# Kernel tuning notes

Measured on AMD Instinct MI355X. Metric: run time of the kernel, lower is better.

## Reference

```python
import jax, jax.numpy as jnp
import numpy as np

EPS = 1e-5


def _ln(x, g, b):
    m = jnp.mean(x, axis=-1, keepdims=True)
    v = jnp.var(x, axis=-1, keepdims=True)
    return (x - m) * jax.lax.rsqrt(v + EPS) * g + b


def setup_inputs() -> dict:
    key = jax.random.key(0)
    B, N, C, H = 1, 384, 128, 128
    ks = jax.random.split(key, 8)

    def lin(k, fan_in, fan_out):
        return (jax.random.normal(k, (fan_in, fan_out), jnp.float32)
                / np.float32(np.sqrt(fan_in)))

    return {
        "pair": jax.random.normal(ks[0], (B, N, N, C), jnp.float32),
        # LayerNorm params
        "g_left": jnp.ones((C,), jnp.float32), "b_left": jnp.zeros((C,), jnp.float32),
        "g_right": jnp.ones((C,), jnp.float32), "b_right": jnp.zeros((C,), jnp.float32),
        "g_out": jnp.ones((C,), jnp.float32), "b_out": jnp.zeros((C,), jnp.float32),
        # Linear params (stored as (in, out))
        "W_l": lin(ks[1], C, H), "bias_l": jnp.zeros((H,), jnp.float32),
        "W_r": lin(ks[2], C, H), "bias_r": jnp.zeros((H,), jnp.float32),
        "W_g": lin(ks[3], C, H), "bias_g": jnp.zeros((H,), jnp.float32),
        "W_e": lin(ks[4], C, H), "bias_e": jnp.zeros((H,), jnp.float32),
        "W_o": lin(ks[5], H, C), "bias_o": jnp.zeros((C,), jnp.float32),
    }


def reference(pair, g_left, b_left, g_right, b_right, g_out, b_out,
              W_l, bias_l, W_r, bias_r, W_g, bias_g, W_e, bias_e,
              W_o, bias_o):
    # pair: (B, N, N, C)
    left = _ln(pair, g_left, b_left) @ W_l + bias_l        # (B,N,N,H)
    right = _ln(pair, g_right, b_right) @ W_r + bias_r     # (B,N,N,H)
    gate = jax.nn.sigmoid(pair @ W_g + bias_g)             # (B,N,N,H)
    left = left + pair @ W_e + bias_e                      # eq branch
    # triangular multiplication: contract over k per hidden channel
    out = jnp.einsum('bikh,bkjh->bijh', left, right)       # (B,N,N,H)
    out = out * gate
    out = out @ W_o + bias_o                               # (B,N,N,C)
    return _ln(out + pair, g_out, b_out)
```

## Files before the change

### kernel.cpp

```cpp
#include <hip/hip_runtime.h>

#define N_  384
#define C_  128
#define NN_ (N_*N_)

typedef __bf16 bf16x8 __attribute__((ext_vector_type(8)));
typedef float  floatx4 __attribute__((ext_vector_type(4)));

__device__ inline unsigned short f2bf(float f) {
    __bf16 h = (__bf16)f;
    return __builtin_bit_cast(unsigned short, h);
}

__global__ void prep(
    const float* __restrict__ Wl, const float* __restrict__ Wr,
    const float* __restrict__ Wg, const float* __restrict__ We,
    const float* __restrict__ gl, const float* __restrict__ bl,
    const float* __restrict__ gr, const float* __restrict__ br,
    const float* __restrict__ bsl, const float* __restrict__ bse,
    const float* __restrict__ bsr,
    __bf16* __restrict__ WtL, __bf16* __restrict__ WtE,
    __bf16* __restrict__ WtR, __bf16* __restrict__ WtG,
    float* __restrict__ cL, float* __restrict__ cR,
    float* __restrict__ sEw, float* __restrict__ sGw)
{
    const int b = blockIdx.x, t = threadIdx.x;
    if (b < 4) {
        const float* W  = (b==0) ? Wl  : (b==1) ? We  : (b==2) ? Wr  : Wg;
        __bf16*      Wt = (b==0) ? WtL : (b==1) ? WtE : (b==2) ? WtR : WtG;
        float scale = (b==0) ? gl[t] : (b==2) ? gr[t] : 1.f;
        for (int h = 0; h < C_; ++h)
            Wt[(size_t)h*C_ + t] = (__bf16)(W[(size_t)t*C_ + h] * scale);
    } else {
        float aL = 0.f, aR = 0.f, aE = 0.f, aG = 0.f;
        for (int c = 0; c < C_; ++c) {
            aL += bl[c] * Wl[(size_t)c*C_ + t];
            aR += br[c] * Wr[(size_t)c*C_ + t];
            aE += We[(size_t)c*C_ + t];
            aG += Wg[(size_t)c*C_ + t];
        }
        cL[t]  = aL + bsl[t] + bse[t];
        cR[t]  = aR + bsr[t];
        sEw[t] = aE;
        sGw[t] = aG;
    }
}

__global__ __launch_bounds__(256) void p_proj(
    const float* __restrict__ pair,
    const __bf16* __restrict__ WtL, const __bf16* __restrict__ WtE,
    const __bf16* __restrict__ WtR, const __bf16* __restrict__ WtG,
    const float* __restrict__ cL, const float* __restrict__ cR,
    const float* __restrict__ sEw, const float* __restrict__ sGw,
    const float* __restrict__ bsg,
    int h0, int nh,
    __bf16* __restrict__ leftC, __bf16* __restrict__ rightC,
    __bf16* __restrict__ gateC)
{
    __shared__ __align__(16) __bf16 sW4[4][32][128];
    __shared__ __align__(16) __bf16 sT3[3][32][72];
    __shared__ float sM[64], sIv[64];

    const int t = threadIdx.x;
    const int rid0 = blockIdx.x * 64;
    const int lane = t & 63, w = t >> 6;
    const int l15 = lane & 15, quad = lane >> 4;

    bf16x8 yf[4];
    {
        const int myrow = w*16 + l15;
        const float* prow = pair + (size_t)(rid0 + myrow)*C_;
        float4 xa[4], xb[4];
        float s = 0.f, sq = 0.f;
        #pragma unroll
        for (int ks = 0; ks < 4; ++ks) {
            xa[ks] = *(const float4*)(prow + ks*32 + quad*8);
            xb[ks] = *(const float4*)(prow + ks*32 + quad*8 + 4);
            s  += xa[ks].x + xa[ks].y + xa[ks].z + xa[ks].w
                + xb[ks].x + xb[ks].y + xb[ks].z + xb[ks].w;
            sq += xa[ks].x*xa[ks].x + xa[ks].y*xa[ks].y
                + xa[ks].z*xa[ks].z + xa[ks].w*xa[ks].w
                + xb[ks].x*xb[ks].x + xb[ks].y*xb[ks].y
                + xb[ks].z*xb[ks].z + xb[ks].w*xb[ks].w;
        }
        s  += __shfl_xor(s, 16);  s  += __shfl_xor(s, 32);
        sq += __shfl_xor(sq, 16); sq += __shfl_xor(sq, 32);
        float m  = s * (1.f/128.f);
        float v  = sq * (1.f/128.f) - m*m;
        float rs = rsqrtf(v + 1e-5f);
        if (quad == 0) { sM[myrow] = m; sIv[myrow] = 1.f / rs; }
        #pragma unroll
        for (int ks = 0; ks < 4; ++ks) {
            yf[ks][0] = (__bf16)((xa[ks].x - m)*rs);
            yf[ks][1] = (__bf16)((xa[ks].y - m)*rs);
            yf[ks][2] = (__bf16)((xa[ks].z - m)*rs);
            yf[ks][3] = (__bf16)((xa[ks].w - m)*rs);
            yf[ks][4] = (__bf16)((xb[ks].x - m)*rs);
            yf[ks][5] = (__bf16)((xb[ks].y - m)*rs);
            yf[ks][6] = (__bf16)((xb[ks].z - m)*rs);
            yf[ks][7] = (__bf16)((xb[ks].w - m)*rs);
        }
    }

    for (int half = 0; half < nh; ++half) {
        const int hb = h0 + half*32;
        {
            const int hh = t >> 3, c8 = t & 7;
            const __bf16* srcs[4] = {
                WtL + (size_t)(hb + hh)*C_, WtE + (size_t)(hb + hh)*C_,
                WtR + (size_t)(hb + hh)*C_, WtG + (size_t)(hb + hh)*C_ };
            #pragma unroll
            for (int mat = 0; mat < 4; ++mat) {
                #pragma unroll
                for (int rep = 0; rep < 2; ++rep) {
                    int cc = c8 + rep*8;
                    *(uint4*)&sW4[mat][hh][((cc ^ (hh & 7)) << 3)] =
                        *(const uint4*)(srcs[mat] + cc*8);
                }
            }
        }
        __syncthreads();

        floatx4 aL[2] = {}, aE[2] = {}, aR[2] = {}, aG[2] = {};
        #pragma unroll
        for (int ks = 0; ks < 4; ++ks) {
            const int cs = ((ks*4 + quad) ^ (l15 & 7)) << 3;
            const bf16x8 af = yf[ks];
            #pragma unroll
            for (int nt = 0; nt < 2; ++nt) {
                const int hr = nt*16 + l15;
                aL[nt] = __builtin_amdgcn_mfma_f32_16x16x32_bf16(
                    af, *(const bf16x8*)&sW4[0][hr][cs], aL[nt], 0, 0, 0);
                aE[nt] = __builtin_amdgcn_mfma_f32_16x16x32_bf16(
                    af, *(const bf16x8*)&sW4[1][hr][cs], aE[nt], 0, 0, 0);
                aR[nt] = __builtin_amdgcn_mfma_f32_16x16x32_bf16(
                    af, *(const bf16x8*)&sW4[2][hr][cs], aR[nt], 0, 0, 0);
                aG[nt] = __builtin_amdgcn_mfma_f32_16x16x32_bf16(
                    af, *(const bf16x8*)&sW4[3][hr][cs], aG[nt], 0, 0, 0);
            }
        }

        #pragma unroll
        for (int nt = 0; nt < 2; ++nt) {
            const int hl_ = nt*16 + l15;
            const float se = sEw[hb + hl_], clv = cL[hb + hl_];
            const float crv = cR[hb + hl_];
            const float sg_ = sGw[hb + hl_], bg = bsg[hb + hl_];
            #pragma unroll
            for (int reg = 0; reg < 4; ++reg) {
                const int rr = w*16 + quad*4 + reg;
                sT3[0][hl_][rr] = (__bf16)(aL[nt][reg] + sIv[rr]*aE[nt][reg]
                                           + sM[rr]*se + clv);
                sT3[1][hl_][rr] = (__bf16)(aR[nt][reg] + crv);
                float z = sIv[rr]*aG[nt][reg] + sM[rr]*sg_ + bg;
                sT3[2][hl_][rr] = (__bf16)(1.f / (1.f + expf(-z)));
            }
        }
        __syncthreads();
        {
            const int hh = t >> 3, sg = t & 7;
            const size_t off = (size_t)(half*32 + hh)*NN_ + rid0 + sg*8;
            *(uint4*)(leftC  + off) = *(const uint4*)&sT3[0][hh][sg*8];
            *(uint4*)(rightC + off) = *(const uint4*)&sT3[1][hh][sg*8];
            *(uint4*)(gateC  + off) = *(const uint4*)&sT3[2][hh][sg*8];
        }
        if (half + 1 < nh) __syncthreads();
    }
}

__global__ __launch_bounds__(256) void t_right(__bf16* __restrict__ p)
{
    __shared__ __align__(16) __bf16 tA[64][72];
    __shared__ __align__(16) __bf16 tB[64][72];
    const int plane = blockIdx.x / 21;
    int rem = blockIdx.x % 21, ri = 0;
    while (rem >= 6 - ri) { rem -= 6 - ri; ++ri; }
    const int ci = ri + rem;
    __bf16* base = p + (size_t)plane * NN_;
    const int t = threadIdx.x;
    const int r = t >> 2, c0 = (t & 3) * 16;

    {
        const __bf16* srcA = base + (size_t)(ri*64 + r)*N_ + ci*64 + c0;
        *(uint4*)&tA[r][c0]   = *(const uint4*)(srcA);
        *(uint4*)&tA[r][c0+8] = *(const uint4*)(srcA + 8);
        if (ri != ci) {
            const __bf16* srcB = base + (size_t)(ci*64 + r)*N_ + ri*64 + c0;
            *(uint4*)&tB[r][c0]   = *(const uint4*)(srcB);
            *(uint4*)&tB[r][c0+8] = *(const uint4*)(srcB + 8);
        }
    }
    __syncthreads();
    {
        union { unsigned short us[8]; uint4 v; } o0, o1;
        #pragma unroll
        for (int u = 0; u < 8; ++u) {
            o0.us[u] = __builtin_bit_cast(unsigned short, tA[c0+u][r]);
            o1.us[u] = __builtin_bit_cast(unsigned short, tA[c0+8+u][r]);
        }
        __bf16* dA = base + (size_t)(ci*64 + r)*N_ + ri*64 + c0;
        *(uint4*)(dA)     = o0.v;
        *(uint4*)(dA + 8) = o1.v;
        if (ri != ci) {
            union { unsigned short us[8]; uint4 v; } p0, p1;
            #pragma unroll
            for (int u = 0; u < 8; ++u) {
                p0.us[u] = __builtin_bit_cast(unsigned short, tB[c0+u][r]);
                p1.us[u] = __builtin_bit_cast(unsigned short, tB[c0+8+u][r]);
            }
            __bf16* dB = base + (size_t)(ri*64 + r)*N_ + ci*64 + c0;
            *(uint4*)(dB)     = p0.v;
            *(uint4*)(dB + 8) = p1.v;
        }
    }
}

__global__ __launch_bounds__(256) void k_einsum(
    const __bf16* __restrict__ leftC, const __bf16* __restrict__ rightC,
    const __bf16* __restrict__ gate, __bf16* __restrict__ outG)
{
    __shared__ __align__(16) unsigned char smem[128*136*2];
    __bf16 (*sA)[40]    = (__bf16(*)[40])smem;
    __bf16 (*sB)[40]    = (__bf16(*)[40])(smem + 128*40*2);
    __bf16 (*sGate)[136] = (__bf16(*)[136])smem;

    const int cpx = gridDim.x >> 3;
    const int bid = (blockIdx.x & 7) * cpx + (blockIdx.x >> 3);
    const int hl = bid / 9, t9 = bid % 9;
    const int ti = (t9 / 3) * 128, tj = (t9 % 3) * 128;
    const int tid = threadIdx.x, lane = tid & 63, w = tid >> 6;
    const int l15 = lane & 15, quad = lane >> 4;
    const size_t hNN = (size_t)hl * NN_;

    const int ar = (lane >> 2);
    const int ac = (lane & 3) * 8;
    const __bf16* gA = leftC  + hNN + (size_t)ti * N_;
    const __bf16* gB = rightC + hNN + (size_t)tj * N_;

    floatx4 acc[4][4] = {};

    for (int ks = 0; ks < 12; ++ks) {
        const int kc = ks * 32;
        uint4 va[2], vb[2];
        #pragma unroll
        for (int it = 0; it < 2; ++it) {
            int row = w*32 + it*16 + ar;
            va[it] = *(const uint4*)(gA + (size_t)row*N_ + kc + ac);
            vb[it] = *(const uint4*)(gB + (size_t)row*N_ + kc + ac);
        }
        #pragma unroll
        for (int it = 0; it < 2; ++it) {
            int row = w*32 + it*16 + ar;
            *(uint4*)&sA[row][ac] = va[it];
            *(uint4*)&sB[row][ac] = vb[it];
        }
        __syncthreads();
        bf16x8 af[4], bfr[4];
        #pragma unroll
        for (int mt = 0; mt < 4; ++mt)
            af[mt] = *(const bf16x8*)&sA[(w&1)*64 + mt*16 + l15][quad*8];
        #pragma unroll
        for (int nt = 0; nt < 4; ++nt)
            bfr[nt] = *(const bf16x8*)&sB[(w>>1)*64 + nt*16 + l15][quad*8];
        #pragma unroll
        for (int mt = 0; mt < 4; ++mt)
            #pragma unroll
            for (int nt = 0; nt < 4; ++nt)
                acc[mt][nt] = __builtin_amdgcn_mfma_f32_16x16x32_bf16(
                    af[mt], bfr[nt], acc[mt][nt], 0, 0, 0);
        __syncthreads();
    }

    #pragma unroll
    for (int it = 0; it < 8; ++it) {
        int cid = it*256 + tid;
        int ri = cid >> 4, c8 = cid & 15;
        *(uint4*)&sGate[ri][c8*8] =
            *(const uint4*)(gate + hNN + (size_t)(ti + ri)*N_ + tj + c8*8);
    }
    __syncthreads();

    const int ib = (w & 1) * 64, jbw = (w >> 1) * 64;
    #pragma unroll
    for (int mt = 0; mt < 4; ++mt) {
        const int i_base = ib + mt*16 + quad*4;
        #pragma unroll
        for (int nt = 0; nt < 4; ++nt) {
            const int j_loc = jbw + nt*16 + l15;
            union { unsigned short us[4]; uint2 v; } p;
            #pragma unroll
            for (int rr = 0; rr < 4; ++rr) {
                float g = (float)sGate[i_base + rr][j_loc];
                p.us[rr] = f2bf(acc[mt][nt][rr] * g);
            }
            *(uint2*)(outG + hNN + (size_t)(tj + j_loc)*N_ + ti + i_base) = p.v;
        }
    }
}

__global__ __launch_bounds__(256) void p_out(
    const __bf16* __restrict__ outG, const float* __restrict__ Wo,
    const float* __restrict__ bso,  const float* __restrict__ pair,
    const float* __restrict__ go,   const float* __restrict__ bo,
    float* __restrict__ out)
{
    __shared__ __align__(16) __bf16 sOh[64][128];
    __shared__ __align__(16) __bf16 sWo[128][128];

    const int t = threadIdx.x;
    const int j  = blockIdx.x / 6;
    const int i0 = (blockIdx.x % 6) * 64;
    const int lane = t & 63, w = t >> 6;
    const int l15 = lane & 15, quad = lane >> 4;

    {
        const int h = t >> 1, ibase = (t & 1) * 32;
        const __bf16* src = outG + (size_t)h*NN_ + (size_t)j*N_ + i0 + ibase;
        #pragma unroll
        for (int u = 0; u < 4; ++u) {
            uint4 vv = *(const uint4*)(src + u*8);
            const unsigned short* pv = (const unsigned short*)&vv;
            #pragma unroll
            for (int k = 0; k < 8; ++k) {
                int i = ibase + u*8 + k;
                sOh[i][(((h >> 3) ^ (i & 7)) << 3) + (h & 7)] =
                    __builtin_bit_cast(__bf16, pv[k]);
            }
        }
    }
    {
        const int h = t >> 1, cbase = (t & 1) * 64;
        const float* src = Wo + (size_t)h*C_ + cbase;
        #pragma unroll
        for (int u = 0; u < 16; ++u) {
            float4 wv = *(const float4*)(src + u*4);
            const float* wf = (const float*)&wv;
            #pragma unroll
            for (int k = 0; k < 4; ++k) {
                int c = cbase + u*4 + k;
                sWo[c][(((h >> 3) ^ (c & 7)) << 3) + (h & 7)] = (__bf16)wf[k];
            }
        }
    }
    __syncthreads();

    floatx4 acc[8] = {};
    #pragma unroll
    for (int ks = 0; ks < 4; ++ks) {
        const int cs = ((ks*4 + quad) ^ (l15 & 7)) << 3;
        bf16x8 af = *(const bf16x8*)&sOh[w*16 + l15][cs];
        #pragma unroll
        for (int nt = 0; nt < 8; ++nt)
            acc[nt] = __builtin_amdgcn_mfma_f32_16x16x32_bf16(
                af, *(const bf16x8*)&sWo[nt*16 + l15][cs], acc[nt], 0, 0, 0);
    }

    float bsov[8], gov[8], bov[8];
    #pragma unroll
    for (int nt = 0; nt < 8; ++nt) {
        const int c = nt*16 + l15;
        bsov[nt] = bso[c]; gov[nt] = go[c]; bov[nt] = bo[c];
    }

    #pragma unroll
    for (int reg = 0; reg < 4; ++reg) {
        const int i = i0 + w*16 + quad*4 + reg;
        const float* prow = pair + ((size_t)i*N_ + j)*C_;
        float zz[8];
        float ssum = 0.f, ssq = 0.f;
        #pragma unroll
        for (int nt = 0; nt < 8; ++nt) {
            float zv = acc[nt][reg] + bsov[nt] + prow[nt*16 + l15];
            zz[nt] = zv; ssum += zv; ssq += zv*zv;
        }
        #pragma unroll
        for (int d = 1; d < 16; d <<= 1) {
            ssum += __shfl_xor(ssum, d);
            ssq  += __shfl_xor(ssq, d);
        }
        const float mm = ssum * (1.f/128.f);
        const float vv = ssq * (1.f/128.f) - mm*mm;
        const float rr = rsqrtf(vv + 1e-5f);
        float* orow = out + ((size_t)i*N_ + j)*C_;
        #pragma unroll
        for (int nt = 0; nt < 8; ++nt)
            orow[nt*16 + l15] = (zz[nt] - mm)*rr*gov[nt] + bov[nt];
    }
}

extern "C" void kernel_launch(void* const* d_in, const int* in_sizes, int n_in,
                              void* d_out, int out_size, void* d_ws, size_t ws_size,
                              hipStream_t stream)
{
    const float* pair    = (const float*)d_in[0];
    const float* g_left  = (const float*)d_in[1];
    const float* b_left  = (const float*)d_in[2];
    const float* g_right = (const float*)d_in[3];
    const float* b_right = (const float*)d_in[4];
    const float* g_out   = (const float*)d_in[5];
    const float* b_out   = (const float*)d_in[6];
    const float* W_l     = (const float*)d_in[7];
    const float* bias_l  = (const float*)d_in[8];
    const float* W_r     = (const float*)d_in[9];
    const float* bias_r  = (const float*)d_in[10];
    const float* W_g     = (const float*)d_in[11];
    const float* bias_g  = (const float*)d_in[12];
    const float* W_e     = (const float*)d_in[13];
    const float* bias_e  = (const float*)d_in[14];
    const float* W_o     = (const float*)d_in[15];
    const float* bias_o  = (const float*)d_in[16];

    const size_t PLANES128 = (size_t)128 * NN_;
    const size_t NEED = PLANES128*2*2 + 65536*2 + 512*4;

    if (ws_size >= NEED) {
        __bf16* leftC  = (__bf16*)d_out;
        __bf16* gateC  = leftC + PLANES128;
        __bf16* rightC = (__bf16*)d_ws;
        __bf16* outG   = rightC + PLANES128;
        char* prepBase = (char*)d_ws + PLANES128*2*2;
        __bf16* WtL = (__bf16*)prepBase;
        __bf16* WtE = WtL + 16384;
        __bf16* WtR = WtL + 32768;
        __bf16* WtG = WtL + 49152;
        float*  cL  = (float*)(WtL + 65536);
        float*  cR  = cL + 128;
        float*  sEw = cL + 256;
        float*  sGw = cL + 384;

        prep<<<5, 128, 0, stream>>>(W_l, W_r, W_g, W_e,
                                    g_left, b_left, g_right, b_right,
                                    bias_l, bias_e, bias_r,
                                    WtL, WtE, WtR, WtG, cL, cR, sEw, sGw);
        p_proj<<<NN_/64, 256, 0, stream>>>(pair, WtL, WtE, WtR, WtG,
                                           cL, cR, sEw, sGw, bias_g,
                                           0, 4, leftC, rightC, gateC);
        t_right<<<128*21, 256, 0, stream>>>(rightC);
        k_einsum<<<128*9, 256, 0, stream>>>(leftC, rightC, gateC, outG);
        p_out<<<2304, 256, 0, stream>>>(outG, W_o, bias_o, pair,
                                        g_out, b_out, (float*)d_out);
    } else {
        __bf16* outG   = (__bf16*)d_ws;
        __bf16* leftC  = (__bf16*)d_out;
        __bf16* rightC = leftC + (size_t)64*NN_;
        __bf16* gateC  = leftC + (size_t)128*NN_;

        char* prepBase = (char*)d_out + ((size_t)60 << 20);
        __bf16* WtL = (__bf16*)prepBase;
        __bf16* WtE = WtL + 16384;
        __bf16* WtR = WtL + 32768;
        __bf16* WtG = WtL + 49152;
        float*  cL  = (float*)(WtL + 65536);
        float*  cR  = cL + 128;
        float*  sEw = cL + 256;
        float*  sGw = cL + 384;

        prep<<<5, 128, 0, stream>>>(W_l, W_r, W_g, W_e,
                                    g_left, b_left, g_right, b_right,
                                    bias_l, bias_e, bias_r,
                                    WtL, WtE, WtR, WtG, cL, cR, sEw, sGw);

        for (int h0 = 0; h0 < 128; h0 += 64) {
            p_proj<<<NN_/64, 256, 0, stream>>>(pair, WtL, WtE, WtR, WtG,
                                               cL, cR, sEw, sGw, bias_g,
                                               h0, 2, leftC, rightC, gateC);
            t_right<<<64*21, 256, 0, stream>>>(rightC);
            k_einsum<<<64*9, 256, 0, stream>>>(leftC, rightC, gateC,
                                               outG + (size_t)h0*NN_);
        }
        p_out<<<2304, 256, 0, stream>>>(outG, W_o, bias_o, pair,
                                        g_out, b_out, (float*)d_out);
    }
}
```

Measured before the change: 293.8 us.

## Prefetch next weight and K-tile loads into registers to overlap with MFMA

In the projection kernel, the weights for the next 32-channel chunk are loaded into registers before the current chunk's MFMAs and written to shared memory after the stores, which removes one barrier per iteration. In the triangular matmul kernel, the global loads for the next K-slice are issued after the barrier and before the MFMA block, so memory latency overlaps with compute. The sigmoid also switches from expf to the faster __expf intrinsic. The cost is extra register pressure, which may lower occupancy, plus slightly reduced accuracy in the sigmoid.

```diff
diff --git a/kernel.cpp b/kernel.cpp
--- a/kernel.cpp
+++ b/kernel.cpp
@@ -46,6 +46,34 @@
     }
 }
 
+__device__ __forceinline__ void loadw(
+    uint4 (&wreg)[8],
+    const __bf16* WtL, const __bf16* WtE,
+    const __bf16* WtR, const __bf16* WtG,
+    int hb, int hh, int c8)
+{
+    const __bf16* srcs[4] = {
+        WtL + (size_t)(hb + hh)*C_, WtE + (size_t)(hb + hh)*C_,
+        WtR + (size_t)(hb + hh)*C_, WtG + (size_t)(hb + hh)*C_ };
+    #pragma unroll
+    for (int mat = 0; mat < 4; ++mat)
+        #pragma unroll
+        for (int rep = 0; rep < 2; ++rep)
+            wreg[mat*2 + rep] = *(const uint4*)(srcs[mat] + (c8 + rep*8)*8);
+}
+
+__device__ __forceinline__ void writew(
+    const uint4 (&wreg)[8], __bf16 (*sW4)[32][128], int hh, int c8)
+{
+    #pragma unroll
+    for (int mat = 0; mat < 4; ++mat)
+        #pragma unroll
+        for (int rep = 0; rep < 2; ++rep) {
+            int cc = c8 + rep*8;
+            *(uint4*)&sW4[mat][hh][((cc ^ (hh & 7)) << 3)] = wreg[mat*2 + rep];
+        }
+}
+
 __global__ __launch_bounds__(256) void p_proj(
     const float* __restrict__ pair,
     const __bf16* __restrict__ WtL, const __bf16* __restrict__ WtE,
@@ -65,6 +93,7 @@
     const int rid0 = blockIdx.x * 64;
     const int lane = t & 63, w = t >> 6;
     const int l15 = lane & 15, quad = lane >> 4;
+    const int shh = t >> 3, sc8 = t & 7;
 
     bf16x8 yf[4];
     {
@@ -102,24 +131,19 @@
         }
     }
 
+    {
+        uint4 w0[8];
+        loadw(w0, WtL, WtE, WtR, WtG, h0, shh, sc8);
+        writew(w0, sW4, shh, sc8);
+    }
+    __syncthreads();
+
+    uint4 wnxt[8];
     for (int half = 0; half < nh; ++half) {
         const int hb = h0 + half*32;
-        {
-            const int hh = t >> 3, c8 = t & 7;
-            const __bf16* srcs[4] = {
-                WtL + (size_t)(hb + hh)*C_, WtE + (size_t)(hb + hh)*C_,
-                WtR + (size_t)(hb + hh)*C_, WtG + (size_t)(hb + hh)*C_ };
-            #pragma unroll
-            for (int mat = 0; mat < 4; ++mat) {
-                #pragma unroll
-                for (int rep = 0; rep < 2; ++rep) {
-                    int cc = c8 + rep*8;
-                    *(uint4*)&sW4[mat][hh][((cc ^ (hh & 7)) << 3)] =
-                        *(const uint4*)(srcs[mat] + cc*8);
-                }
-            }
-        }
-        __syncthreads();
+
+        if (half + 1 < nh)
+            loadw(wnxt, WtL, WtE, WtR, WtG, h0 + (half+1)*32, shh, sc8);
 
         floatx4 aL[2] = {}, aE[2] = {}, aR[2] = {}, aG[2] = {};
         #pragma unroll
@@ -153,18 +177,20 @@
                                            + sM[rr]*se + clv);
                 sT3[1][hl_][rr] = (__bf16)(aR[nt][reg] + crv);
                 float z = sIv[rr]*aG[nt][reg] + sM[rr]*sg_ + bg;
-                sT3[2][hl_][rr] = (__bf16)(1.f / (1.f + expf(-z)));
+                sT3[2][hl_][rr] = (__bf16)(1.f / (1.f + __expf(-z)));
             }
         }
         __syncthreads();
         {
-            const int hh = t >> 3, sg = t & 7;
-            const size_t off = (size_t)(half*32 + hh)*NN_ + rid0 + sg*8;
-            *(uint4*)(leftC  + off) = *(const uint4*)&sT3[0][hh][sg*8];
-            *(uint4*)(rightC + off) = *(const uint4*)&sT3[1][hh][sg*8];
-            *(uint4*)(gateC  + off) = *(const uint4*)&sT3[2][hh][sg*8];
-        }
-        if (half + 1 < nh) __syncthreads();
+            const size_t off = (size_t)(half*32 + shh)*NN_ + rid0 + sc8*8;
+            *(uint4*)(leftC  + off) = *(const uint4*)&sT3[0][shh][sc8*8];
+            *(uint4*)(rightC + off) = *(const uint4*)&sT3[1][shh][sc8*8];
+            *(uint4*)(gateC  + off) = *(const uint4*)&sT3[2][shh][sc8*8];
+        }
+        if (half + 1 < nh) {
+            writew(wnxt, sW4, shh, sc8);
+            __syncthreads();
+        }
     }
 }
 
@@ -239,15 +265,15 @@
 
     floatx4 acc[4][4] = {};
 
+    uint4 va[2], vb[2];
+    #pragma unroll
+    for (int it = 0; it < 2; ++it) {
+        int row = w*32 + it*16 + ar;
+        va[it] = *(const uint4*)(gA + (size_t)row*N_ + ac);
+        vb[it] = *(const uint4*)(gB + (size_t)row*N_ + ac);
+    }
+
     for (int ks = 0; ks < 12; ++ks) {
-        const int kc = ks * 32;
-        uint4 va[2], vb[2];
-        #pragma unroll
-        for (int it = 0; it < 2; ++it) {
-            int row = w*32 + it*16 + ar;
-            va[it] = *(const uint4*)(gA + (size_t)row*N_ + kc + ac);
-            vb[it] = *(const uint4*)(gB + (size_t)row*N_ + kc + ac);
-        }
         #pragma unroll
         for (int it = 0; it < 2; ++it) {
             int row = w*32 + it*16 + ar;
@@ -255,6 +281,18 @@
             *(uint4*)&sB[row][ac] = vb[it];
         }
         __syncthreads();
+
+        uint4 va2[2], vb2[2];
+        if (ks + 1 < 12) {
+            const int kc = (ks + 1) * 32;
+            #pragma unroll
+            for (int it = 0; it < 2; ++it) {
+                int row = w*32 + it*16 + ar;
+                va2[it] = *(const uint4*)(gA + (size_t)row*N_ + kc + ac);
+                vb2[it] = *(const uint4*)(gB + (size_t)row*N_ + kc + ac);
+            }
+        }
+
         bf16x8 af[4], bfr[4];
         #pragma unroll
         for (int mt = 0; mt < 4; ++mt)
@@ -269,6 +307,11 @@
                 acc[mt][nt] = __builtin_amdgcn_mfma_f32_16x16x32_bf16(
                     af[mt], bfr[nt], acc[mt][nt], 0, 0, 0);
         __syncthreads();
+
+        if (ks + 1 < 12) {
+            #pragma unroll
+            for (int it = 0; it < 2; ++it) { va[it] = va2[it]; vb[it] = vb2[it]; }
+        }
     }
 
     #pragma unroll
```

Result: slower. 444.9 us (+51.4%).
